# Performance work log

Hardware: AMD Instinct MI355X
Metric: run time of the kernel (lower is better)

The kernel has to match this reference:

```python
import jax, jax.numpy as jnp
import numpy as np

M = 50000   # eval points
N = 1024    # gaussians
EPS = 1e-6


def setup_inputs() -> dict:
    key = jax.random.key(0)
    k1, k2, k3 = jax.random.split(key, 3)
    points = jax.random.uniform(k1, (M, 3), dtype=jnp.float32)          # normalized coords in [0,1)
    positions = jax.random.uniform(k2, (N, 3), dtype=jnp.float32)       # torch.rand init
    log_scales = jnp.full((N, 3), -3.0, dtype=jnp.float32)              # torch.full(..., -3.0)
    intensities = jax.random.uniform(k3, (N,), dtype=jnp.float32) * 0.5  # torch.rand * 0.5
    return {"points": points, "positions": positions,
            "log_scales": log_scales, "intensities": intensities}


def reference(points, positions, log_scales, intensities):
    # Faithful translation of FastGaussianModel._eval_gaussians
    scales = jnp.exp(log_scales)                      # [N,3]
    inv_var = 1.0 / (scales ** 2 + EPS)               # [N,3]
    diff = points[:, None, :] - positions[None, :, :] # [M,N,3]
    quad = jnp.einsum('mnd,nd->mn', diff * diff, inv_var)  # [M,N]
    gauss = jnp.exp(-0.5 * quad)                      # [M,N]
    values = gauss @ intensities                      # [M]
    return values
```

## Files before the change

### kernel.cpp

```cpp
#include <hip/hip_runtime.h>


typedef float v2f __attribute__((ext_vector_type(2)));

constexpr int BLOCK         = 128;
constexpr int WAVES_PER_BLK = 2;
constexpr int PTS_PER_LANE  = 4;
constexpr int TILE_PTS      = 64 * PTS_PER_LANE;
constexpr int SLICE_GROUPS  = 16;
constexpr int TOTAL_SLICES  = SLICE_GROUPS * WAVES_PER_BLK;
constexpr int HDR           = 16;
constexpr int FASTREC       = 12;
constexpr int FULLREC       = 16;


__global__ void fgm_prep(const float* __restrict__ positions,
                         const float* __restrict__ log_scales,
                         const float* __restrict__ intensities,
                         float* __restrict__ ws,
                         float* __restrict__ out, int out_n,
                         int N, int NpairsPad) {
    __shared__ int smismatch;
    if (threadIdx.x == 0) smismatch = 0;
    __syncthreads();

    {
        float4 z = make_float4(0.f, 0.f, 0.f, 0.f);
        float4* o4 = (float4*)out;
        int n4 = out_n >> 2;
        for (int i = threadIdx.x; i < n4; i += blockDim.x) o4[i] = z;
        for (int i = (n4 << 2) + threadIdx.x; i < out_n; i += blockDim.x) out[i] = 0.f;
    }

    const float K = -0.7213475204444817f;
    float r0 = K / (__expf(2.0f*log_scales[0]) + 1e-6f);
    float r1 = K / (__expf(2.0f*log_scales[1]) + 1e-6f);
    float r2 = K / (__expf(2.0f*log_scales[2]) + 1e-6f);

    int mism = 0;
    float* fastT = ws + HDR;
    float* fullT = ws + HDR + (size_t)NpairsPad * FASTREC;
    for (int i = threadIdx.x; i < NpairsPad; i += blockDim.x) {
        float v[2][8];
        for (int h = 0; h < 2; ++h) {
            int n = 2*i + h;
            float a0=0.f,a1=0.f,a2=0.f,b0=0.f,b1=0.f,b2=0.f,c=0.f,w=0.f;
            if (n < N) {
                float q0 = positions[3*n+0], q1 = positions[3*n+1], q2 = positions[3*n+2];
                b0 = K / (__expf(2.0f*log_scales[3*n+0]) + 1e-6f);
                b1 = K / (__expf(2.0f*log_scales[3*n+1]) + 1e-6f);
                b2 = K / (__expf(2.0f*log_scales[3*n+2]) + 1e-6f);
                a0 = -2.f*b0*q0;  a1 = -2.f*b1*q1;  a2 = -2.f*b2*q2;
                c  = b0*q0*q0 + b1*q1*q1 + b2*q2*q2;
                w  = intensities[n];
                if (b0 != r0 || b1 != r1 || b2 != r2) mism = 1;
            }
            v[h][0]=a0; v[h][1]=a1; v[h][2]=a2; v[h][3]=b0;
            v[h][4]=b1; v[h][5]=b2; v[h][6]=c;  v[h][7]=w;
        }
        float4* f = (float4*)(fastT + (size_t)i * FASTREC);
        f[0] = make_float4(v[0][0], v[1][0], v[0][1], v[1][1]);
        f[1] = make_float4(v[0][2], v[1][2], v[0][6], v[1][6]);
        f[2] = make_float4(v[0][7], v[1][7], 0.f,     0.f);
        float4* o = (float4*)(fullT + (size_t)i * FULLREC);
        o[0] = make_float4(v[0][0], v[1][0], v[0][1], v[1][1]);
        o[1] = make_float4(v[0][2], v[1][2], v[0][3], v[1][3]);
        o[2] = make_float4(v[0][4], v[1][4], v[0][5], v[1][5]);
        o[3] = make_float4(v[0][6], v[1][6], v[0][7], v[1][7]);
    }
    if (mism) atomicOr(&smismatch, 1);
    __syncthreads();
    if (threadIdx.x == 0) {
        ws[0] = smismatch ? 1.f : 0.f;
        ws[1] = r0;  ws[2] = r1;  ws[3] = r2;
    }
}

template <int PAIRS>
__device__ __forceinline__ void sweep_fast(const v2f* __restrict__ cp, int pairs,
                                           const float* px, const float* py,
                                           const float* pz, const float* pp,
                                           v2f* acc) {
    const int n = PAIRS > 0 ? PAIRS : pairs;
    #pragma unroll
    for (int i = 0; i < n; ++i) {
        v2f A0 = cp[0], A1 = cp[1], A2 = cp[2], C = cp[3], W = cp[4];
        cp += 6;
        #pragma unroll
        for (int j = 0; j < PTS_PER_LANE; ++j) {
            v2f t = C + (v2f){pp[j], pp[j]};
            t = __builtin_elementwise_fma(A2, (v2f){pz[j], pz[j]}, t);
            t = __builtin_elementwise_fma(A1, (v2f){py[j], py[j]}, t);
            t = __builtin_elementwise_fma(A0, (v2f){px[j], px[j]}, t);
            v2f g;
            g.x = __builtin_amdgcn_exp2f(t.x);
            g.y = __builtin_amdgcn_exp2f(t.y);
            acc[j] = __builtin_elementwise_fma(g, W, acc[j]);
        }
    }
}

__device__ __forceinline__ void sweep_full(const v2f* __restrict__ cp, int pairs,
                                           const float* px, const float* py,
                                           const float* pz, v2f* acc) {
    #pragma unroll 2
    for (int i = 0; i < pairs; ++i) {
        v2f A0 = cp[0], A1 = cp[1], A2 = cp[2];
        v2f B0 = cp[3], B1 = cp[4], B2 = cp[5];
        v2f C  = cp[6], W  = cp[7];
        cp += 8;
        #pragma unroll
        for (int j = 0; j < PTS_PER_LANE; ++j) {
            v2f t = __builtin_elementwise_fma(B0, (v2f){px[j]*px[j], px[j]*px[j]}, C);
            t = __builtin_elementwise_fma(B1, (v2f){py[j]*py[j], py[j]*py[j]}, t);
            t = __builtin_elementwise_fma(B2, (v2f){pz[j]*pz[j], pz[j]*pz[j]}, t);
            t = __builtin_elementwise_fma(A2, (v2f){pz[j], pz[j]}, t);
            t = __builtin_elementwise_fma(A1, (v2f){py[j], py[j]}, t);
            t = __builtin_elementwise_fma(A0, (v2f){px[j], px[j]}, t);
            v2f g;
            g.x = __builtin_amdgcn_exp2f(t.x);
            g.y = __builtin_amdgcn_exp2f(t.y);
            acc[j] = __builtin_elementwise_fma(g, W, acc[j]);
        }
    }
}

template <int PAIRS>
__global__ __launch_bounds__(BLOCK) void fgm_main(const float* __restrict__ points,
                                                  const float* __restrict__ ws,
                                                  float* __restrict__ out,
                                                  int M, int pairsPerSlice,
                                                  int NpairsPad) {
    __shared__ float red[WAVES_PER_BLK][TILE_PTS];

    int lane = threadIdx.x & 63;
    int wave = __builtin_amdgcn_readfirstlane(threadIdx.x >> 6);
    int tileBase = blockIdx.x * TILE_PTS;
    int slice = blockIdx.y * WAVES_PER_BLK + wave;

    bool fast = (ws[0] == 0.f);
    float hb0 = ws[1], hb1 = ws[2], hb2 = ws[3];

    float px[PTS_PER_LANE], py[PTS_PER_LANE], pz[PTS_PER_LANE], pp[PTS_PER_LANE];
    v2f acc[PTS_PER_LANE];
    #pragma unroll
    for (int j = 0; j < PTS_PER_LANE; ++j) {
        int m = tileBase + lane + 64*j;
        float x = 0.f, y = 0.f, z = 0.f;
        if (m < M) { x = points[3*m+0]; y = points[3*m+1]; z = points[3*m+2]; }
        px[j] = x;  py[j] = y;  pz[j] = z;
        pp[j] = hb0*x*x + hb1*y*y + hb2*z*z;
        acc[j] = (v2f){0.f, 0.f};
    }

    if (fast) {
        const v2f* cp = (const v2f*)(ws + HDR) + (size_t)slice * pairsPerSlice * 6;
        sweep_fast<PAIRS>(cp, pairsPerSlice, px, py, pz, pp, acc);
    } else {
        const v2f* cp = (const v2f*)(ws + HDR + (size_t)NpairsPad * FASTREC)
                        + (size_t)slice * pairsPerSlice * 8;
        sweep_full(cp, pairsPerSlice, px, py, pz, acc);
    }

    #pragma unroll
    for (int j = 0; j < PTS_PER_LANE; ++j)
        red[wave][lane + 64*j] = acc[j].x + acc[j].y;
    __syncthreads();

    for (int p = threadIdx.x; p < TILE_PTS; p += BLOCK) {
        int m = tileBase + p;
        if (m < M) atomicAdd(&out[m], red[0][p] + red[1][p]);
    }
}

extern "C" void kernel_launch(void* const* d_in, const int* in_sizes, int n_in,
                              void* d_out, int out_size, void* d_ws, size_t ws_size,
                              hipStream_t stream) {
    const float* points      = (const float*)d_in[0];
    const float* positions   = (const float*)d_in[1];
    const float* log_scales  = (const float*)d_in[2];
    const float* intensities = (const float*)d_in[3];
    int M = in_sizes[0] / 3;
    int N = in_sizes[3];

    int Npairs        = (N + 1) / 2;
    int pairsPerSlice = (Npairs + TOTAL_SLICES - 1) / TOTAL_SLICES;
    int NpairsPad     = pairsPerSlice * TOTAL_SLICES;

    float* ws = (float*)d_ws;

    fgm_prep<<<1, 256, 0, stream>>>(positions, log_scales, intensities,
                                    ws, (float*)d_out, out_size, N, NpairsPad);

    int tiles = (M + TILE_PTS - 1) / TILE_PTS;
    dim3 grid(tiles, SLICE_GROUPS);
    if (pairsPerSlice == 16) {
        fgm_main<16><<<grid, BLOCK, 0, stream>>>(points, ws, (float*)d_out,
                                                 M, pairsPerSlice, NpairsPad);
    } else {
        fgm_main<0><<<grid, BLOCK, 0, stream>>>(points, ws, (float*)d_out,
                                                M, pairsPerSlice, NpairsPad);
    }
}
```

Measured before the change: 75.70 us.

## Fuse Gaussian parameter prep into main kernel via per-wave LDS records

Removes the single-block prep kernel that wrote coefficient tables to workspace. Each wave now computes its own slice's Gaussian coefficients directly into shared memory, checks for uniform scales with a wave vote, and zeroes the output with a memset. It also doubles the slice groups so each wave handles 8 pairs instead of 16. This cuts the serial single-block prep launch and the dependency it creates, in exchange for redundant per-block coefficient computation (exp and divide) and twice as many atomic adds to the output.

```diff
diff --git a/kernel.cpp b/kernel.cpp
--- a/kernel.cpp
+++ b/kernel.cpp
@@ -7,74 +7,13 @@
 constexpr int WAVES_PER_BLK = 2;
 constexpr int PTS_PER_LANE  = 4;
 constexpr int TILE_PTS      = 64 * PTS_PER_LANE;
-constexpr int SLICE_GROUPS  = 16;
+constexpr int SLICE_GROUPS  = 32;
 constexpr int TOTAL_SLICES  = SLICE_GROUPS * WAVES_PER_BLK;
-constexpr int HDR           = 16;
-constexpr int FASTREC       = 12;
-constexpr int FULLREC       = 16;
+constexpr int RECF          = 16;
+constexpr int MAXPPS        = 48;
+constexpr float KLN  = -0.7213475204444817f;
+constexpr float FEPS = 1e-6f;
 
-
-__global__ void fgm_prep(const float* __restrict__ positions,
-                         const float* __restrict__ log_scales,
-                         const float* __restrict__ intensities,
-                         float* __restrict__ ws,
-                         float* __restrict__ out, int out_n,
-                         int N, int NpairsPad) {
-    __shared__ int smismatch;
-    if (threadIdx.x == 0) smismatch = 0;
-    __syncthreads();
-
-    {
-        float4 z = make_float4(0.f, 0.f, 0.f, 0.f);
-        float4* o4 = (float4*)out;
-        int n4 = out_n >> 2;
-        for (int i = threadIdx.x; i < n4; i += blockDim.x) o4[i] = z;
-        for (int i = (n4 << 2) + threadIdx.x; i < out_n; i += blockDim.x) out[i] = 0.f;
-    }
-
-    const float K = -0.7213475204444817f;
-    float r0 = K / (__expf(2.0f*log_scales[0]) + 1e-6f);
-    float r1 = K / (__expf(2.0f*log_scales[1]) + 1e-6f);
-    float r2 = K / (__expf(2.0f*log_scales[2]) + 1e-6f);
-
-    int mism = 0;
-    float* fastT = ws + HDR;
-    float* fullT = ws + HDR + (size_t)NpairsPad * FASTREC;
-    for (int i = threadIdx.x; i < NpairsPad; i += blockDim.x) {
-        float v[2][8];
-        for (int h = 0; h < 2; ++h) {
-            int n = 2*i + h;
-            float a0=0.f,a1=0.f,a2=0.f,b0=0.f,b1=0.f,b2=0.f,c=0.f,w=0.f;
-            if (n < N) {
-                float q0 = positions[3*n+0], q1 = positions[3*n+1], q2 = positions[3*n+2];
-                b0 = K / (__expf(2.0f*log_scales[3*n+0]) + 1e-6f);
-                b1 = K / (__expf(2.0f*log_scales[3*n+1]) + 1e-6f);
-                b2 = K / (__expf(2.0f*log_scales[3*n+2]) + 1e-6f);
-                a0 = -2.f*b0*q0;  a1 = -2.f*b1*q1;  a2 = -2.f*b2*q2;
-                c  = b0*q0*q0 + b1*q1*q1 + b2*q2*q2;
-                w  = intensities[n];
-                if (b0 != r0 || b1 != r1 || b2 != r2) mism = 1;
-            }
-            v[h][0]=a0; v[h][1]=a1; v[h][2]=a2; v[h][3]=b0;
-            v[h][4]=b1; v[h][5]=b2; v[h][6]=c;  v[h][7]=w;
-        }
-        float4* f = (float4*)(fastT + (size_t)i * FASTREC);
-        f[0] = make_float4(v[0][0], v[1][0], v[0][1], v[1][1]);
-        f[1] = make_float4(v[0][2], v[1][2], v[0][6], v[1][6]);
-        f[2] = make_float4(v[0][7], v[1][7], 0.f,     0.f);
-        float4* o = (float4*)(fullT + (size_t)i * FULLREC);
-        o[0] = make_float4(v[0][0], v[1][0], v[0][1], v[1][1]);
-        o[1] = make_float4(v[0][2], v[1][2], v[0][3], v[1][3]);
-        o[2] = make_float4(v[0][4], v[1][4], v[0][5], v[1][5]);
-        o[3] = make_float4(v[0][6], v[1][6], v[0][7], v[1][7]);
-    }
-    if (mism) atomicOr(&smismatch, 1);
-    __syncthreads();
-    if (threadIdx.x == 0) {
-        ws[0] = smismatch ? 1.f : 0.f;
-        ws[1] = r0;  ws[2] = r1;  ws[3] = r2;
-    }
-}
 
 template <int PAIRS>
 __device__ __forceinline__ void sweep_fast(const v2f* __restrict__ cp, int pairs,
@@ -85,7 +24,7 @@
     #pragma unroll
     for (int i = 0; i < n; ++i) {
         v2f A0 = cp[0], A1 = cp[1], A2 = cp[2], C = cp[3], W = cp[4];
-        cp += 6;
+        cp += 8;
         #pragma unroll
         for (int j = 0; j < PTS_PER_LANE; ++j) {
             v2f t = C + (v2f){pp[j], pp[j]};
@@ -100,14 +39,15 @@
     }
 }
 
+template <int PAIRS>
 __device__ __forceinline__ void sweep_full(const v2f* __restrict__ cp, int pairs,
                                            const float* px, const float* py,
                                            const float* pz, v2f* acc) {
+    const int n = PAIRS > 0 ? PAIRS : pairs;
     #pragma unroll 2
-    for (int i = 0; i < pairs; ++i) {
-        v2f A0 = cp[0], A1 = cp[1], A2 = cp[2];
-        v2f B0 = cp[3], B1 = cp[4], B2 = cp[5];
-        v2f C  = cp[6], W  = cp[7];
+    for (int i = 0; i < n; ++i) {
+        v2f A0 = cp[0], A1 = cp[1], A2 = cp[2], C = cp[3], W = cp[4];
+        v2f B0 = cp[5], B1 = cp[6], B2 = cp[7];
         cp += 8;
         #pragma unroll
         for (int j = 0; j < PTS_PER_LANE; ++j) {
@@ -126,40 +66,78 @@
 }
 
 template <int PAIRS>
-__global__ __launch_bounds__(BLOCK) void fgm_main(const float* __restrict__ points,
-                                                  const float* __restrict__ ws,
-                                                  float* __restrict__ out,
-                                                  int M, int pairsPerSlice,
-                                                  int NpairsPad) {
+__global__ __launch_bounds__(BLOCK) void fgm_main(
+        const float* __restrict__ points,
+        const float* __restrict__ positions,
+        const float* __restrict__ log_scales,
+        const float* __restrict__ intensities,
+        float* __restrict__ out,
+        int M, int N, int pairsPerSlice) {
+    constexpr int CPAIRS = PAIRS > 0 ? PAIRS : MAXPPS;
+    __shared__ __align__(16) float recs[WAVES_PER_BLK][CPAIRS * RECF];
     __shared__ float red[WAVES_PER_BLK][TILE_PTS];
 
-    int lane = threadIdx.x & 63;
-    int wave = __builtin_amdgcn_readfirstlane(threadIdx.x >> 6);
-    int tileBase = blockIdx.x * TILE_PTS;
-    int slice = blockIdx.y * WAVES_PER_BLK + wave;
+    const int lane = threadIdx.x & 63;
+    const int wave = __builtin_amdgcn_readfirstlane(threadIdx.x >> 6);
+    const int tileBase = blockIdx.x * TILE_PTS;
+    const int slice = blockIdx.y * WAVES_PER_BLK + wave;
+    const int PPS = PAIRS > 0 ? PAIRS : pairsPerSlice;
 
-    bool fast = (ws[0] == 0.f);
-    float hb0 = ws[1], hb1 = ws[2], hb2 = ws[3];
+    const float r0 = KLN / (__expf(2.0f * log_scales[0]) + FEPS);
+    const float r1 = KLN / (__expf(2.0f * log_scales[1]) + FEPS);
+    const float r2 = KLN / (__expf(2.0f * log_scales[2]) + FEPS);
 
     float px[PTS_PER_LANE], py[PTS_PER_LANE], pz[PTS_PER_LANE], pp[PTS_PER_LANE];
     v2f acc[PTS_PER_LANE];
     #pragma unroll
     for (int j = 0; j < PTS_PER_LANE; ++j) {
-        int m = tileBase + lane + 64*j;
+        int m = tileBase + lane + 64 * j;
         float x = 0.f, y = 0.f, z = 0.f;
         if (m < M) { x = points[3*m+0]; y = points[3*m+1]; z = points[3*m+2]; }
         px[j] = x;  py[j] = y;  pz[j] = z;
-        pp[j] = hb0*x*x + hb1*y*y + hb2*z*z;
+        pp[j] = r0*x*x + r1*y*y + r2*z*z;
         acc[j] = (v2f){0.f, 0.f};
     }
 
-    if (fast) {
-        const v2f* cp = (const v2f*)(ws + HDR) + (size_t)slice * pairsPerSlice * 6;
-        sweep_fast<PAIRS>(cp, pairsPerSlice, px, py, pz, pp, acc);
-    } else {
-        const v2f* cp = (const v2f*)(ws + HDR + (size_t)NpairsPad * FASTREC)
-                        + (size_t)slice * pairsPerSlice * 8;
-        sweep_full(cp, pairsPerSlice, px, py, pz, acc);
+    for (int base = 0; base < PPS; base += CPAIRS) {
+        const int cnt = (PPS - base < CPAIRS) ? (PPS - base) : CPAIRS;
+
+        bool ok = true;
+        for (int p = lane; p < cnt; p += 64) {
+            float va[2][8];
+            #pragma unroll
+            for (int h = 0; h < 2; ++h) {
+                int n = (slice * PPS + base + p) * 2 + h;
+                float a0=0.f,a1=0.f,a2=0.f,b0=0.f,b1=0.f,b2=0.f,c=0.f,w=0.f;
+                if (n < N) {
+                    float q0 = positions[3*n+0], q1 = positions[3*n+1], q2 = positions[3*n+2];
+                    b0 = KLN / (__expf(2.0f*log_scales[3*n+0]) + FEPS);
+                    b1 = KLN / (__expf(2.0f*log_scales[3*n+1]) + FEPS);
+                    b2 = KLN / (__expf(2.0f*log_scales[3*n+2]) + FEPS);
+                    a0 = -2.f*b0*q0;  a1 = -2.f*b1*q1;  a2 = -2.f*b2*q2;
+                    c  = b0*q0*q0 + b1*q1*q1 + b2*q2*q2;
+                    w  = intensities[n];
+                    if (b0 != r0 || b1 != r1 || b2 != r2) ok = false;
+                }
+                va[h][0]=a0; va[h][1]=a1; va[h][2]=a2; va[h][3]=b0;
+                va[h][4]=b1; va[h][5]=b2; va[h][6]=c;  va[h][7]=w;
+            }
+            v2f* r = (v2f*)&recs[wave][p * RECF];
+            r[0] = (v2f){va[0][0], va[1][0]};
+            r[1] = (v2f){va[0][1], va[1][1]};
+            r[2] = (v2f){va[0][2], va[1][2]};
+            r[3] = (v2f){va[0][6], va[1][6]};
+            r[4] = (v2f){va[0][7], va[1][7]};
+            r[5] = (v2f){va[0][3], va[1][3]};
+            r[6] = (v2f){va[0][4], va[1][4]};
+            r[7] = (v2f){va[0][5], va[1][5]};
+        }
+        const bool fast = __all(ok);
+        __syncthreads();
+
+        const v2f* cp = (const v2f*)recs[wave];
+        if (fast) sweep_fast<PAIRS>(cp, cnt, px, py, pz, pp, acc);
+        else      sweep_full<PAIRS>(cp, cnt, px, py, pz, acc);
     }
 
     #pragma unroll
@@ -183,22 +161,18 @@
     int M = in_sizes[0] / 3;
     int N = in_sizes[3];
 
-    int Npairs        = (N + 1) / 2;
-    int pairsPerSlice = (Npairs + TOTAL_SLICES - 1) / TOTAL_SLICES;
-    int NpairsPad     = pairsPerSlice * TOTAL_SLICES;
+    int Npairs = (N + 1) / 2;
+    int PPS    = (Npairs + TOTAL_SLICES - 1) / TOTAL_SLICES;
 
-    float* ws = (float*)d_ws;
-
-    fgm_prep<<<1, 256, 0, stream>>>(positions, log_scales, intensities,
-                                    ws, (float*)d_out, out_size, N, NpairsPad);
+    hipMemsetAsync(d_out, 0, (size_t)out_size * sizeof(float), stream);
 
     int tiles = (M + TILE_PTS - 1) / TILE_PTS;
     dim3 grid(tiles, SLICE_GROUPS);
-    if (pairsPerSlice == 16) {
-        fgm_main<16><<<grid, BLOCK, 0, stream>>>(points, ws, (float*)d_out,
-                                                 M, pairsPerSlice, NpairsPad);
+    if (PPS == 8) {
+        fgm_main<8><<<grid, BLOCK, 0, stream>>>(points, positions, log_scales,
+                                                intensities, (float*)d_out, M, N, PPS);
     } else {
-        fgm_main<0><<<grid, BLOCK, 0, stream>>>(points, ws, (float*)d_out,
-                                                M, pairsPerSlice, NpairsPad);
+        fgm_main<0><<<grid, BLOCK, 0, stream>>>(points, positions, log_scales,
+                                                intensities, (float*)d_out, M, N, PPS);
     }
 }
```

Result: no change. 75.14 us (-0.7%).
